# Optimization experiments

Hardware: AMD Instinct MI355X
Metric: run time of the kernel (lower is better)

## Reference

```python
import jax, jax.numpy as jnp
import numpy as np

N_HEAD = 16
N_KV_HEADS = 4
N_REP = 4
HEAD_DIM = 128
N_EMBD = 2048
EPS = 1e-5
ROPE_BASE = 10000.0


def setup_inputs() -> dict:
    key = jax.random.key(0)
    ks = jax.random.split(key, 5)
    B, T, C = 2, 2048, N_EMBD
    s = 0.02
    return {
        "x": jax.random.normal(ks[0], (B, T, C), dtype=jnp.float32),
        "wq": jax.random.normal(ks[1], (C, N_HEAD * HEAD_DIM), dtype=jnp.float32) * s,
        "wk": jax.random.normal(ks[2], (C, N_KV_HEADS * HEAD_DIM), dtype=jnp.float32) * s,
        "wv": jax.random.normal(ks[3], (C, N_KV_HEADS * HEAD_DIM), dtype=jnp.float32) * s,
        "wc": jax.random.normal(ks[4], (C, C), dtype=jnp.float32) * s,
        "q_norm_w": jnp.ones((HEAD_DIM,), dtype=jnp.float32),
        "k_norm_w": jnp.ones((HEAD_DIM,), dtype=jnp.float32),
    }


def _rmsnorm(x, w):
    # norm in fp32, scale by weight (matches RMSNorm.forward)
    xf = x.astype(jnp.float32)
    rms = jax.lax.rsqrt(jnp.mean(xf * xf, axis=-1, keepdims=True) + EPS)
    return (xf * rms).astype(x.dtype) * w


def _rope(x, cos, sin):
    # x: [B,T,H,D]; cos/sin: [T, D//2]; interleaved even/odd rotation
    xf = x.astype(jnp.float32)
    xe = xf[..., 0::2]
    xo = xf[..., 1::2]
    c = cos[None, :, None, :]
    s = sin[None, :, None, :]
    ye = xe * c - xo * s
    yo = xe * s + xo * c
    y = jnp.stack((ye, yo), axis=-1).reshape(x.shape)
    return y.astype(x.dtype)


def reference(x, wq, wk, wv, wc, q_norm_w, k_norm_w):
    B, T, C = x.shape
    q = (x @ wq).reshape(B, T, N_HEAD, HEAD_DIM)
    k = (x @ wk).reshape(B, T, N_KV_HEADS, HEAD_DIM)
    v = (x @ wv).reshape(B, T, N_KV_HEADS, HEAD_DIM)

    q = _rmsnorm(q, q_norm_w)
    k = _rmsnorm(k, k_norm_w)

    inv_freq = 1.0 / (ROPE_BASE ** (jnp.arange(0, HEAD_DIM, 2, dtype=jnp.float32) / HEAD_DIM))
    theta = jnp.arange(T, dtype=jnp.float32)[:, None] * inv_freq[None, :]  # [T, D//2]
    cos, sin = jnp.cos(theta), jnp.sin(theta)
    q = _rope(q, cos, sin)
    k = _rope(k, cos, sin)

    # GQA: repeat kv heads (repeat_kv with n_rep)
    k = jnp.repeat(k, N_REP, axis=2)  # [B,T,H,D]
    v = jnp.repeat(v, N_REP, axis=2)

    scale = 1.0 / jnp.sqrt(jnp.float32(HEAD_DIM))
    scores = jnp.einsum("bthd,bshd->bhts", q, k) * scale  # [B,H,T,S]
    causal = jnp.tril(jnp.ones((T, T), dtype=bool))
    scores = jnp.where(causal[None, None], scores, jnp.finfo(scores.dtype).min)
    attn = jax.nn.softmax(scores, axis=-1)
    y = jnp.einsum("bhts,bshd->bthd", attn, v).reshape(B, T, C)
    return y @ wc
```

## Files before the change

### kernel.cpp

```cpp
#include <hip/hip_runtime.h>
#include <hip/hip_bf16.h>
#include <cstdint>
#include <cstddef>

using bf16 = __hip_bfloat16;
typedef __attribute__((ext_vector_type(8))) short short8;
typedef __attribute__((ext_vector_type(4))) float f32x4;
typedef __attribute__((ext_vector_type(16))) float f32x16;

#define T_SEQ 2048
#define NHEAD 16
#define NKV 4
#define HD 128
#define CE 2048

__device__ __forceinline__ void gl_lds16(const void* g, void* l) {
  __builtin_amdgcn_global_load_lds(
      (const __attribute__((address_space(1))) unsigned int*)g,
      (__attribute__((address_space(3))) unsigned int*)l, 16, 0, 0);
}

__device__ __forceinline__ unsigned int cvtpk_bf16(float lo, float hi) {
  unsigned int r;
  asm("v_cvt_pk_bf16_f32 %0, %1, %2" : "=v"(r) : "v"(lo), "v"(hi));
  return r;
}

__device__ __forceinline__ void plswap(unsigned int& x, unsigned int& y, int hi) {
#if __has_builtin(__builtin_amdgcn_permlane32_swap)
  auto r = __builtin_amdgcn_permlane32_swap(x, y, false, false);
  x = r[0];
  y = r[1];
#else
  unsigned int xp = (unsigned int)__shfl_xor((int)x, 32);
  unsigned int yp = (unsigned int)__shfl_xor((int)y, 32);
  unsigned int nx = hi ? yp : x;
  unsigned int ny = hi ? y : xp;
  x = nx;
  y = ny;
#endif
}

__global__ void __launch_bounds__(256) cvt_bf16(const float* __restrict__ in,
                                                bf16* __restrict__ out, int n4) {
  const int i = blockIdx.x * blockDim.x + threadIdx.x;
  if (i >= n4) return;
  const float4 v = ((const float4*)in)[i];
  bf16 b0 = __float2bfloat16(v.x), b1 = __float2bfloat16(v.y),
       b2 = __float2bfloat16(v.z), b3 = __float2bfloat16(v.w);
  ushort4 u;
  u.x = *(const unsigned short*)&b0; u.y = *(const unsigned short*)&b1;
  u.z = *(const unsigned short*)&b2; u.w = *(const unsigned short*)&b3;
  ((ushort4*)out)[i] = u;
}

__global__ void __launch_bounds__(256) transpose_cvt(const float* __restrict__ W,
                                                     bf16* __restrict__ Wt, int N) {
  __shared__ float tile[32][33];
  const int tx = threadIdx.x & 31, ty = threadIdx.x >> 5;
  const int bx = blockIdx.x, by = blockIdx.y;
#pragma unroll
  for (int i = 0; i < 4; i++) {
    const int r = by * 32 + ty + i * 8;
    tile[ty + i * 8][tx] = W[(size_t)r * N + bx * 32 + tx];
  }
  __syncthreads();
#pragma unroll
  for (int i = 0; i < 4; i++) {
    const int n = bx * 32 + ty + i * 8;
    Wt[(size_t)n * 2048 + by * 32 + tx] = __float2bfloat16(tile[tx][ty + i * 8]);
  }
}

template <int BM, int BN, int WM, int WN, bool OBF>
__global__ void __launch_bounds__(512, 2)
gemm4p(const bf16* __restrict__ A, const bf16* __restrict__ Bt,
       void* __restrict__ Cv, int M, int N, int K) {
  constexpr int AWS = BM / 2 / WM;
  constexpr int BWS = BN / 2 / WN;
  constexpr int MH = AWS / 16;
  constexpr int NH = BWS / 16;
  constexpr int AL = BM / 64;
  constexpr int BL = BN / 64;
  constexpr int AH = AL / 2;
  constexpr int BH = BL / 2;
  constexpr int G1N = AH + (BH + AH);
  constexpr int G2N = BH;
  __shared__ bf16 smA[2][BM * 64];
  __shared__ bf16 smB[2][BN * 64];

  const int tid = threadIdx.x, lane = tid & 63, wid = tid >> 6;
  const int l15 = lane & 15, l4 = lane >> 4;
  const int wr = wid / WN, wc = wid % WN;

  const int nwg = gridDim.x;
  const int q = nwg >> 3, r = nwg & 7;
  const int xcd = blockIdx.x & 7, lin = blockIdx.x >> 3;
  const int wg = (xcd < r ? xcd * (q + 1) : r * (q + 1) + (xcd - r) * q) + lin;
  const int gw = N / BN;
  const int by = wg / gw, bx = wg % gw;
  const int row0 = by * BM, col0 = bx * BN;
  const int NT = K >> 6;

  const bf16* Ag = A + (size_t)row0 * K;
  const bf16* Bg = Bt + (size_t)col0 * K;

  auto stA = [&](int t, int h, int pb) {
    const int k0 = t << 6;
#pragma unroll
    for (int j = 0; j < AH; j++) {
      const int c = (h * AH + j) * 512 + tid;
      const int rowi = c >> 3;
      gl_lds16(Ag + (size_t)rowi * K + k0 + (((c & 7) ^ (rowi & 7)) << 3),
               (void*)(&smA[pb][(size_t)c << 3]));
    }
  };
  auto stB = [&](int t, int h, int pb) {
    const int k0 = t << 6;
#pragma unroll
    for (int j = 0; j < BH; j++) {
      const int c = (h * BH + j) * 512 + tid;
      const int rowi = c >> 3;
      gl_lds16(Bg + (size_t)rowi * K + k0 + (((c & 7) ^ (rowi & 7)) << 3),
               (void*)(&smB[pb][(size_t)c << 3]));
    }
  };
  auto rdA = [&](const bf16* sA, int mh, short8 (&dst)[MH][2]) {
#pragma unroll
    for (int i = 0; i < MH; i++) {
      const int rowl = mh * (BM / 2) + wr * AWS + i * 16 + l15;
#pragma unroll
      for (int kk = 0; kk < 2; kk++)
        dst[i][kk] = *(const short8*)(sA + rowl * 64 +
                                      ((((kk << 2) | l4) ^ (rowl & 7)) << 3));
    }
  };
  auto rdB = [&](const bf16* sB, int nh, short8 (&dst)[NH][2]) {
#pragma unroll
    for (int j = 0; j < NH; j++) {
      const int rowl = nh * (BN / 2) + wc * BWS + j * 16 + l15;
#pragma unroll
      for (int kk = 0; kk < 2; kk++)
        dst[j][kk] = *(const short8*)(sB + rowl * 64 +
                                      ((((kk << 2) | l4) ^ (rowl & 7)) << 3));
    }
  };

  f32x4 acc[2][2][MH][NH];
#pragma unroll
  for (int mh = 0; mh < 2; mh++)
#pragma unroll
    for (int nh = 0; nh < 2; nh++)
#pragma unroll
      for (int i = 0; i < MH; i++)
#pragma unroll
        for (int j = 0; j < NH; j++) acc[mh][nh][i][j] = (f32x4){0.f, 0.f, 0.f, 0.f};

  auto mmq = [&](short8 (&a)[MH][2], short8 (&b)[NH][2], f32x4 (&ac)[MH][NH]) {
    __builtin_amdgcn_s_setprio(1);
#pragma unroll
    for (int i = 0; i < MH; i++)
#pragma unroll
      for (int j = 0; j < NH; j++)
#pragma unroll
        for (int kk = 0; kk < 2; kk++)
          ac[i][j] = __builtin_amdgcn_mfma_f32_16x16x32_bf16(a[i][kk], b[j][kk],
                                                             ac[i][j], 0, 0, 0);
    __builtin_amdgcn_s_setprio(0);
  };

  short8 a0[MH][2], a1[MH][2], b0[NH][2], b1[NH][2];

  stA(0, 0, 0); stA(0, 1, 0); stB(0, 0, 0); stB(0, 1, 0);
  asm volatile("s_waitcnt vmcnt(0)" ::: "memory");
  __builtin_amdgcn_s_barrier();

  for (int t = 0; t < NT; ++t) {
    const int buf = t & 1;
    const bf16* sA = smA[buf];
    const bf16* sB = smB[buf];
    const int tn = (t + 1 < NT) ? t + 1 : t;

    stA(tn, 0, buf ^ 1);
    rdA(sA, 0, a0);
    rdB(sB, 0, b0);
    __builtin_amdgcn_s_barrier();
    asm volatile("s_waitcnt lgkmcnt(0)" ::: "memory");
    __builtin_amdgcn_sched_barrier(0);
    mmq(a0, b0, acc[0][0]);
    __builtin_amdgcn_s_barrier();
    stB(tn, 0, buf ^ 1);
    stA(tn, 1, buf ^ 1);
    rdA(sA, 1, a1);
    __builtin_amdgcn_s_barrier();
    asm volatile("s_waitcnt lgkmcnt(0)" ::: "memory");
    __builtin_amdgcn_sched_barrier(0);
    mmq(a1, b0, acc[1][0]);
    asm volatile("s_waitcnt vmcnt(%0)" ::"i"(G1N) : "memory");
    __builtin_amdgcn_s_barrier();
    stB(tn, 1, buf ^ 1);
    rdB(sB, 1, b1);
    __builtin_amdgcn_s_barrier();
    asm volatile("s_waitcnt lgkmcnt(0)" ::: "memory");
    __builtin_amdgcn_sched_barrier(0);
    mmq(a1, b1, acc[1][1]);
    __builtin_amdgcn_s_barrier();
    mmq(a0, b1, acc[0][1]);
    asm volatile("s_waitcnt vmcnt(%0)" ::"i"(G2N) : "memory");
    __builtin_amdgcn_s_barrier();
  }

#pragma unroll
  for (int mh = 0; mh < 2; mh++)
#pragma unroll
    for (int nh = 0; nh < 2; nh++)
#pragma unroll
      for (int i = 0; i < MH; i++)
#pragma unroll
        for (int j = 0; j < NH; j++)
#pragma unroll
          for (int rr = 0; rr < 4; rr++) {
            const size_t row = row0 + mh * (BM / 2) + wr * AWS + i * 16 + l4 * 4 + rr;
            const size_t col = col0 + nh * (BN / 2) + wc * BWS + j * 16 + l15;
            if constexpr (OBF)
              ((bf16*)Cv)[row * N + col] = __float2bfloat16(acc[mh][nh][i][j][rr]);
            else
              ((float*)Cv)[row * N + col] = acc[mh][nh][i][j][rr];
          }

  asm volatile("s_waitcnt vmcnt(0)" ::: "memory");
}

__global__ void __launch_bounds__(256) qkv_post(const bf16* __restrict__ QKV,
                                                const float* __restrict__ qw,
                                                const float* __restrict__ kw,
                                                bf16* __restrict__ Qo,
                                                bf16* __restrict__ Ko,
                                                bf16* __restrict__ Vto) {
  const int g = blockIdx.x * 4 + (threadIdx.x >> 6);
  const int lane = threadIdx.x & 63;
  const int hh = g % 24;
  const int bt = g / 24;
  const int b = bt >> 11, t = bt & (T_SEQ - 1);
  int off;
  if (hh < 16) off = hh * 128;
  else if (hh < 20) off = 2048 + (hh - 16) * 128;
  else off = 2560 + (hh - 20) * 128;
  const ushort2 xr = *(const ushort2*)(QKV + (size_t)bt * 3072 + off + lane * 2);
  const float xx = __bfloat162float(*(const bf16*)&xr.x);
  const float xy = __bfloat162float(*(const bf16*)&xr.y);
  if (hh < 20) {
    float ss = xx * xx + xy * xy;
    ss += __shfl_xor(ss, 1);  ss += __shfl_xor(ss, 2);  ss += __shfl_xor(ss, 4);
    ss += __shfl_xor(ss, 8);  ss += __shfl_xor(ss, 16); ss += __shfl_xor(ss, 32);
    const float rms = rsqrtf(ss * (1.0f / 128.0f) + 1e-5f);
    const float* w = (hh < 16) ? qw : kw;
    const float x0 = xx * rms * w[lane * 2];
    const float x1 = xy * rms * w[lane * 2 + 1];
    const float inv = exp2f((float)lane * (-13.287712379549449f / 64.0f));
    const float th = (float)t * inv;
    const float sn = sinf(th), cs = cosf(th);
    const float y0 = x0 * cs - x1 * sn;
    const float y1 = x0 * sn + x1 * cs;
    const bf16 o0 = __float2bfloat16(y0), o1 = __float2bfloat16(y1);
    if (hh < 16) {
      bf16* d = Qo + ((size_t)(b * NHEAD + hh) * T_SEQ + t) * HD + lane * 2;
      d[0] = o0; d[1] = o1;
    } else {
      bf16* d = Ko + ((size_t)(b * NKV + (hh - 16)) * T_SEQ + t) * HD + lane * 2;
      d[0] = o0; d[1] = o1;
    }
  } else {
    bf16* d = Vto + ((size_t)(b * NKV + (hh - 20)) * HD + lane * 2) * T_SEQ + t;
    d[0] = __float2bfloat16(xx);
    d[T_SEQ] = __float2bfloat16(xy);
  }
}

__global__ void __launch_bounds__(256, 2) attn_fwd(const bf16* __restrict__ Q,
                                                   const bf16* __restrict__ K,
                                                   const bf16* __restrict__ Vt,
                                                   bf16* __restrict__ Y) {
  __shared__ bf16 smK[128 * 128];
  __shared__ bf16 smV[128 * 128];

  const int bid = blockIdx.x;
  const int p = bid & 255, sdx = bid >> 8;
  const int bh = p & 31;
  const int jh = p >> 5;
  const int jq = sdx ? (15 - jh) : jh;
  const int h = bh & (NHEAD - 1), b = bh >> 4;
  const int bkv = b * NKV + (h >> 2);

  const int tid = threadIdx.x, wid = tid >> 6, lane = tid & 63;
  const int l31 = lane & 31, hi = lane >> 5;
  const int q0w = jq * 128 + wid * 32;

  const bf16* Kb = K + (size_t)bkv * T_SEQ * HD;
  const bf16* Vb = Vt + (size_t)bkv * HD * T_SEQ;

  const bf16* Qrow = Q + ((size_t)bh * T_SEQ + q0w + l31) * HD + hi * 8;
  short8 qf[8];
#pragma unroll
  for (int ds = 0; ds < 8; ds++) qf[ds] = *(const short8*)(Qrow + ds * 16);

  f32x16 o[4];
#pragma unroll
  for (int d = 0; d < 4; d++) o[d] = (f32x16)(0.f);
  float mrun = -INFINITY, lrun = 0.f;

  constexpr float CL = 0.08838834764831845f * 1.44269504088896340736f;
  const int trow = tid >> 4, tslot = tid & 15;

  for (int t = 0; t <= jq; t++) {
    const int k0 = t * 128;
    __syncthreads();
#pragma unroll
    for (int i = 0; i < 8; i++) {
      const int row = i * 16 + trow;
      const int ss = (tslot ^ (row & 15)) * 8;
      gl_lds16(Kb + (size_t)(k0 + row) * HD + ss, (void*)((char*)smK + i * 4096 + wid * 1024));
      gl_lds16(Vb + (size_t)row * T_SEQ + k0 + ss, (void*)((char*)smV + i * 4096 + wid * 1024));
    }
    __syncthreads();

    const bool lastt = (t == jq);
    const int glim = lastt ? wid : 3;

    f32x16 sg[4];
#pragma unroll
    for (int g = 0; g < 4; g++) {
      if (g > glim) continue;
      f32x16 acc = (f32x16)(0.f);
#pragma unroll
      for (int ds = 0; ds < 8; ds++) {
        const int row = g * 32 + l31;
        const short8 kf = *(const short8*)(smK + (size_t)row * 128 +
                                           (((ds << 1) | hi) ^ (row & 15)) * 8);
        acc = __builtin_amdgcn_mfma_f32_32x32x16_bf16(kf, qf[ds], acc, 0, 0, 0);
      }
      sg[g] = acc;
    }
    float tmax = -INFINITY;
#pragma unroll
    for (int g = 0; g < 4; g++) {
      if (g > glim) continue;
      if (lastt && g == wid) {
#pragma unroll
        for (int r = 0; r < 16; r++) {
          const int kr = (r & 3) + 8 * (r >> 2) + (hi << 2);
          if (kr > l31) sg[g][r] = -INFINITY;
        }
      }
#pragma unroll
      for (int r = 0; r < 16; r++) tmax = fmaxf(tmax, sg[g][r]);
    }
    tmax = fmaxf(tmax, __shfl_xor(tmax, 32));
    const float mnew = fmaxf(mrun, tmax);
    const float f = exp2f((mrun - mnew) * CL);
    mrun = mnew;
    lrun *= f;
#pragma unroll
    for (int d = 0; d < 4; d++)
#pragma unroll
      for (int r = 0; r < 16; r++) o[d][r] *= f;

    float lsum = 0.f;
#pragma unroll
    for (int g = 0; g < 4; g++) {
      if (g > glim) continue;
      float pp[16];
      float s0 = 0.f, s1 = 0.f;
#pragma unroll
      for (int r = 0; r < 16; r++) pp[r] = exp2f((sg[g][r] - mnew) * CL);
#pragma unroll
      for (int r = 0; r < 8; r++) { s0 += pp[2 * r]; s1 += pp[2 * r + 1]; }
      lsum += s0 + s1;

      unsigned int w0 = cvtpk_bf16(pp[0], pp[1]),  w2 = cvtpk_bf16(pp[4], pp[5]);
      unsigned int w1 = cvtpk_bf16(pp[2], pp[3]),  w3 = cvtpk_bf16(pp[6], pp[7]);
      unsigned int w4 = cvtpk_bf16(pp[8], pp[9]),  w6 = cvtpk_bf16(pp[12], pp[13]);
      unsigned int w5 = cvtpk_bf16(pp[10], pp[11]), w7 = cvtpk_bf16(pp[14], pp[15]);
      plswap(w0, w2, hi); plswap(w1, w3, hi);
      plswap(w4, w6, hi); plswap(w5, w7, hi);
      union { unsigned int u[4]; short8 s8; } pa0, pa1;
      pa0.u[0] = w0; pa0.u[1] = w1; pa0.u[2] = w2; pa0.u[3] = w3;
      pa1.u[0] = w4; pa1.u[1] = w5; pa1.u[2] = w6; pa1.u[3] = w7;

#pragma unroll
      for (int d = 0; d < 4; d++) {
        const int row = d * 32 + l31;
        const int ks0 = g * 2, ks1 = g * 2 + 1;
        const short8 vf0 = *(const short8*)(smV + (size_t)row * 128 +
                                            (((ks0 << 1) | hi) ^ (row & 15)) * 8);
        const short8 vf1 = *(const short8*)(smV + (size_t)row * 128 +
                                            (((ks1 << 1) | hi) ^ (row & 15)) * 8);
        o[d] = __builtin_amdgcn_mfma_f32_32x32x16_bf16(vf0, pa0.s8, o[d], 0, 0, 0);
        o[d] = __builtin_amdgcn_mfma_f32_32x32x16_bf16(vf1, pa1.s8, o[d], 0, 0, 0);
      }
    }
    lrun += lsum + __shfl_xor(lsum, 32);
  }

  const float inv = 1.0f / lrun;
  bf16* yrow = Y + ((size_t)(b * T_SEQ + q0w + l31)) * CE + h * HD;
#pragma unroll
  for (int d = 0; d < 4; d++) {
#pragma unroll
    for (int rg = 0; rg < 4; rg++) {
      ushort4 u;
      bf16 e0 = __float2bfloat16(o[d][rg * 4 + 0] * inv);
      bf16 e1 = __float2bfloat16(o[d][rg * 4 + 1] * inv);
      bf16 e2 = __float2bfloat16(o[d][rg * 4 + 2] * inv);
      bf16 e3 = __float2bfloat16(o[d][rg * 4 + 3] * inv);
      u.x = *(const unsigned short*)&e0; u.y = *(const unsigned short*)&e1;
      u.z = *(const unsigned short*)&e2; u.w = *(const unsigned short*)&e3;
      *(ushort4*)(yrow + d * 32 + rg * 8 + (hi << 2)) = u;
    }
  }
}

extern "C" void kernel_launch(void* const* d_in, const int* in_sizes, int n_in,
                              void* d_out, int out_size, void* d_ws, size_t ws_size,
                              hipStream_t stream) {
  const float* x   = (const float*)d_in[0];
  const float* wq  = (const float*)d_in[1];
  const float* wk  = (const float*)d_in[2];
  const float* wv  = (const float*)d_in[3];
  const float* wc  = (const float*)d_in[4];
  const float* qnw = (const float*)d_in[5];
  const float* knw = (const float*)d_in[6];
  float* out = (float*)d_out;

  char* ws = (char*)d_ws;
  bf16*  xb    = (bf16*)(ws);
  bf16*  wqkvt = (bf16*)(ws + 16777216);
  bf16*  wct   = (bf16*)(ws + 29360128);
  bf16*  qkv   = (bf16*)(ws + 37748736);
  bf16*  Qb    = (bf16*)(ws + 88080384);
  bf16*  Kb    = (bf16*)(ws + 104857600);
  bf16*  Vtb   = (bf16*)(ws + 109051904);
  bf16*  yb    = (bf16*)(ws + 113246208);

  cvt_bf16<<<8192, 256, 0, stream>>>(x, xb, 2097152);
  transpose_cvt<<<dim3(64, 64), 256, 0, stream>>>(wq, wqkvt, 2048);
  transpose_cvt<<<dim3(16, 64), 256, 0, stream>>>(wk, wqkvt + (size_t)2048 * 2048, 512);
  transpose_cvt<<<dim3(16, 64), 256, 0, stream>>>(wv, wqkvt + (size_t)2560 * 2048, 512);
  transpose_cvt<<<dim3(64, 64), 256, 0, stream>>>(wc, wct, 2048);
  gemm4p<256, 256, 2, 4, true><<<192, 512, 0, stream>>>(xb, wqkvt, qkv, 4096, 3072, 2048);
  qkv_post<<<24576, 256, 0, stream>>>(qkv, qnw, knw, Qb, Kb, Vtb);
  attn_fwd<<<512, 256, 0, stream>>>(Qb, Kb, Vtb, yb);
  gemm4p<128, 256, 2, 4, false><<<256, 512, 0, stream>>>(yb, wct, out, 4096, 2048, 2048);
}
```

Baseline: 254.4 us.

## Unroll GEMM main loop by two with deeper cross-iteration prefetch pipeline

Replaces the GEMM main loop with one unrolled by two. The loop now prefetches the tile two steps ahead into the same LDS buffer as soon as each quarter has been consumed, instead of loading one step ahead into the alternate buffer. This keeps more global loads in flight and uses fixed buffer indices, which removes the per-iteration buffer arithmetic and reduces stalls on vmcnt. The cost is a longer, more complex schedule with a separate epilogue and a risk of LDS hazards if the barrier ordering is wrong.

New measurement: 228.2 us. -10.3%, faster.

```diff
diff --git a/kernel.cpp b/kernel.cpp
--- a/kernel.cpp
+++ b/kernel.cpp
@@ -74,18 +74,15 @@
 
 template <int BM, int BN, int WM, int WN, bool OBF>
 __global__ void __launch_bounds__(512, 2)
-gemm4p(const bf16* __restrict__ A, const bf16* __restrict__ Bt,
+gemm8i(const bf16* __restrict__ A, const bf16* __restrict__ Bt,
        void* __restrict__ Cv, int M, int N, int K) {
   constexpr int AWS = BM / 2 / WM;
   constexpr int BWS = BN / 2 / WN;
   constexpr int MH = AWS / 16;
   constexpr int NH = BWS / 16;
-  constexpr int AL = BM / 64;
-  constexpr int BL = BN / 64;
-  constexpr int AH = AL / 2;
-  constexpr int BH = BL / 2;
-  constexpr int G1N = AH + (BH + AH);
-  constexpr int G2N = BH;
+  constexpr int AH = BM / 128;
+  constexpr int BH = BN / 128;
+  constexpr int G = 2 * AH + BH;
   __shared__ bf16 smA[2][BM * 64];
   __shared__ bf16 smB[2][BN * 64];
 
@@ -101,6 +98,7 @@
   const int by = wg / gw, bx = wg % gw;
   const int row0 = by * BM, col0 = bx * BN;
   const int NT = K >> 6;
+  const int NI = NT >> 1;
 
   const bf16* Ag = A + (size_t)row0 * K;
   const bf16* Bg = Bt + (size_t)col0 * K;
@@ -171,43 +169,100 @@
 
   short8 a0[MH][2], a1[MH][2], b0[NH][2], b1[NH][2];
 
-  stA(0, 0, 0); stA(0, 1, 0); stB(0, 0, 0); stB(0, 1, 0);
-  asm volatile("s_waitcnt vmcnt(0)" ::: "memory");
+#define LGKM0_SB                                            \
+  asm volatile("s_waitcnt lgkmcnt(0)" ::: "memory");        \
+  __builtin_amdgcn_sched_barrier(0);
+#define GATE_G                                              \
+  asm volatile("s_waitcnt vmcnt(%0)" ::"i"(G) : "memory");
+
+  stA(0, 0, 0); stB(0, 0, 0); stA(0, 1, 0); stB(0, 1, 0);
+  stA(1, 0, 1); stB(1, 0, 1); stA(1, 1, 1);
+  GATE_G
   __builtin_amdgcn_s_barrier();
 
-  for (int t = 0; t < NT; ++t) {
-    const int buf = t & 1;
-    const bf16* sA = smA[buf];
-    const bf16* sB = smB[buf];
-    const int tn = (t + 1 < NT) ? t + 1 : t;
-
-    stA(tn, 0, buf ^ 1);
-    rdA(sA, 0, a0);
-    rdB(sB, 0, b0);
-    __builtin_amdgcn_s_barrier();
-    asm volatile("s_waitcnt lgkmcnt(0)" ::: "memory");
-    __builtin_amdgcn_sched_barrier(0);
+  for (int i = 0; i < NI - 1; ++i) {
+    const int u = 2 * i, v = u + 1;
+    stB(v, 1, 1);
+    rdA(smA[0], 0, a0); rdB(smB[0], 0, b0);
+    __builtin_amdgcn_s_barrier();
+    LGKM0_SB
     mmq(a0, b0, acc[0][0]);
     __builtin_amdgcn_s_barrier();
-    stB(tn, 0, buf ^ 1);
-    stA(tn, 1, buf ^ 1);
-    rdA(sA, 1, a1);
-    __builtin_amdgcn_s_barrier();
-    asm volatile("s_waitcnt lgkmcnt(0)" ::: "memory");
-    __builtin_amdgcn_sched_barrier(0);
+    stA(u + 2, 0, 0);
+    rdA(smA[0], 1, a1);
+    __builtin_amdgcn_s_barrier();
+    LGKM0_SB
     mmq(a1, b0, acc[1][0]);
-    asm volatile("s_waitcnt vmcnt(%0)" ::"i"(G1N) : "memory");
-    __builtin_amdgcn_s_barrier();
-    stB(tn, 1, buf ^ 1);
-    rdB(sB, 1, b1);
-    __builtin_amdgcn_s_barrier();
-    asm volatile("s_waitcnt lgkmcnt(0)" ::: "memory");
-    __builtin_amdgcn_sched_barrier(0);
+    __builtin_amdgcn_s_barrier();
+    stB(u + 2, 0, 0);
+    rdB(smB[0], 1, b1);
+    __builtin_amdgcn_s_barrier();
+    LGKM0_SB
     mmq(a1, b1, acc[1][1]);
     __builtin_amdgcn_s_barrier();
+    stA(u + 2, 1, 0);
     mmq(a0, b1, acc[0][1]);
-    asm volatile("s_waitcnt vmcnt(%0)" ::"i"(G2N) : "memory");
-    __builtin_amdgcn_s_barrier();
+    GATE_G
+    __builtin_amdgcn_s_barrier();
+    stB(u + 2, 1, 0);
+    rdA(smA[1], 0, a0); rdB(smB[1], 0, b0);
+    __builtin_amdgcn_s_barrier();
+    LGKM0_SB
+    mmq(a0, b0, acc[0][0]);
+    __builtin_amdgcn_s_barrier();
+    stA(v + 2, 0, 1);
+    rdA(smA[1], 1, a1);
+    __builtin_amdgcn_s_barrier();
+    LGKM0_SB
+    mmq(a1, b0, acc[1][0]);
+    __builtin_amdgcn_s_barrier();
+    stB(v + 2, 0, 1);
+    rdB(smB[1], 1, b1);
+    __builtin_amdgcn_s_barrier();
+    LGKM0_SB
+    mmq(a1, b1, acc[1][1]);
+    __builtin_amdgcn_s_barrier();
+    stA(v + 2, 1, 1);
+    mmq(a0, b1, acc[0][1]);
+    GATE_G
+    __builtin_amdgcn_s_barrier();
+  }
+
+  {
+    stB(NT - 1, 1, 1);
+    rdA(smA[0], 0, a0); rdB(smB[0], 0, b0);
+    __builtin_amdgcn_s_barrier();
+    LGKM0_SB
+    mmq(a0, b0, acc[0][0]);
+    __builtin_amdgcn_s_barrier();
+    rdA(smA[0], 1, a1);
+    __builtin_amdgcn_s_barrier();
+    LGKM0_SB
+    mmq(a1, b0, acc[1][0]);
+    __builtin_amdgcn_s_barrier();
+    rdB(smB[0], 1, b1);
+    __builtin_amdgcn_s_barrier();
+    LGKM0_SB
+    mmq(a1, b1, acc[1][1]);
+    __builtin_amdgcn_s_barrier();
+    mmq(a0, b1, acc[0][1]);
+    asm volatile("s_waitcnt vmcnt(0)" ::: "memory");
+    __builtin_amdgcn_s_barrier();
+    rdA(smA[1], 0, a0); rdB(smB[1], 0, b0);
+    __builtin_amdgcn_s_barrier();
+    LGKM0_SB
+    mmq(a0, b0, acc[0][0]);
+    __builtin_amdgcn_s_barrier();
+    rdA(smA[1], 1, a1);
+    __builtin_amdgcn_s_barrier();
+    LGKM0_SB
+    mmq(a1, b0, acc[1][0]);
+    __builtin_amdgcn_s_barrier();
+    rdB(smB[1], 1, b1);
+    __builtin_amdgcn_s_barrier();
+    LGKM0_SB
+    mmq(a1, b1, acc[1][1]);
+    mmq(a0, b1, acc[0][1]);
   }
 
 #pragma unroll
@@ -227,8 +282,8 @@
             else
               ((float*)Cv)[row * N + col] = acc[mh][nh][i][j][rr];
           }
-
-  asm volatile("s_waitcnt vmcnt(0)" ::: "memory");
+#undef LGKM0_SB
+#undef GATE_G
 }
 
 __global__ void __launch_bounds__(256) qkv_post(const bf16* __restrict__ QKV,
@@ -447,8 +502,8 @@
   transpose_cvt<<<dim3(16, 64), 256, 0, stream>>>(wk, wqkvt + (size_t)2048 * 2048, 512);
   transpose_cvt<<<dim3(16, 64), 256, 0, stream>>>(wv, wqkvt + (size_t)2560 * 2048, 512);
   transpose_cvt<<<dim3(64, 64), 256, 0, stream>>>(wc, wct, 2048);
-  gemm4p<256, 256, 2, 4, true><<<192, 512, 0, stream>>>(xb, wqkvt, qkv, 4096, 3072, 2048);
+  gemm8i<256, 256, 2, 4, true><<<192, 512, 0, stream>>>(xb, wqkvt, qkv, 4096, 3072, 2048);
   qkv_post<<<24576, 256, 0, stream>>>(qkv, qnw, knw, Qb, Kb, Vtb);
   attn_fwd<<<512, 256, 0, stream>>>(Qb, Kb, Vtb, yb);
-  gemm4p<128, 256, 2, 4, false><<<256, 512, 0, stream>>>(yb, wct, out, 4096, 2048, 2048);
-}
+  gemm8i<128, 256, 2, 4, false><<<256, 512, 0, stream>>>(yb, wct, out, 4096, 2048, 2048);
+}
```
